# Kernel optimization log

Measured on AMD Instinct MI355X. Metric: run time of the kernel, lower is better.

The kernel has to match this reference:

```python
import jax, jax.numpy as jnp
import numpy as np

B, CIN, W = 4, 3, 28          # batch, in_channels, image size (= max_pos_embedding)
MID, HEADS, G, COUT = 16, 8, 4, 64
HALF = MID // 2               # row / col embedding dims


def _embed(u, w1, b1, gamma, beta, w2, b2):
    """Positional-embedding MLP applied elementwise to scalars u (N,).
    Conv2d(1->16,k=1) -> LayerNorm(16 channels) -> Swish -> Conv2d(16->MID/2,k=1)."""
    h = u[:, None] * w1[None, :] + b1                     # (N, 16)
    mu = h.mean(-1, keepdims=True)
    var = ((h - mu) ** 2).mean(-1, keepdims=True)
    h = gamma * (h - mu) / jnp.sqrt(var + 1e-5) + beta    # LayerNorm over channels
    h = h * jax.nn.sigmoid(h)                             # Swish
    return h @ w2.T + b2                                  # (N, HALF)


def _rot_indices():
    """Acted relative-position lookup indices for the 4 rotations.
    Values index into u = concat(rel, -rel) where rel = linspace(-1,1,2W-1)."""
    n = 2 * W - 1
    ar = np.arange(W)
    rel = ar[None, :] - ar[:, None] + (W - 1)             # rel[i,k] in [0, 2W-2]
    R = np.broadcast_to(rel[:, None, :, None], (W,) * 4)  # depends on (i,k)
    C = np.broadcast_to(rel[None, :, None, :], (W,) * 4)  # depends on (j,l)
    # rotation by 0/90/180/270 deg acting on (row, col) relative coordinates
    ridx = np.stack([R, C + n, R + n, C], 0)              # row component index
    cidx = np.stack([C, R, C + n, R + n], 0)              # col component index
    return jnp.asarray(ridx, jnp.int32), jnp.asarray(cidx, jnp.int32)


def setup_inputs() -> dict:
    key = jax.random.key(0)
    ks = jax.random.split(key, 24)
    def nrm(k, shape, fan):
        return jax.random.normal(k, shape, jnp.float32) / np.float32(np.sqrt(fan))
    inp = {"x": jax.random.normal(ks[0], (B, CIN, W, W), jnp.float32)}
    inp["wq"] = nrm(ks[1], (MID * HEADS, CIN), CIN); inp["bq"] = jnp.zeros((MID * HEADS,), jnp.float32)
    inp["wk"] = nrm(ks[2], (MID * HEADS, CIN), CIN); inp["bk"] = jnp.zeros((MID * HEADS,), jnp.float32)
    inp["wv"] = nrm(ks[3], (MID * HEADS, CIN), CIN); inp["bv"] = jnp.zeros((MID * HEADS,), jnp.float32)
    inp["w_out"] = nrm(ks[4], (COUT, MID * HEADS), MID * HEADS); inp["b_out"] = jnp.zeros((COUT,), jnp.float32)
    for pfx, base in (("row", 5), ("col", 12)):
        inp[f"{pfx}_w1"] = nrm(ks[base], (16,), 1)
        inp[f"{pfx}_b1"] = jnp.zeros((16,), jnp.float32)
        inp[f"{pfx}_gamma"] = jnp.ones((16,), jnp.float32)
        inp[f"{pfx}_beta"] = jnp.zeros((16,), jnp.float32)
        inp[f"{pfx}_w2"] = nrm(ks[base + 1], (HALF, 16), 16)
        inp[f"{pfx}_b2"] = jnp.zeros((HALF,), jnp.float32)
    inp["ridx"], inp["cidx"] = _rot_indices()
    return inp


def reference(x, wq, bq, wk, bk, wv, bv, w_out, b_out,
              row_w1, row_b1, row_gamma, row_beta, row_w2, row_b2,
              col_w1, col_b1, col_gamma, col_beta, col_w2, col_b2,
              ridx, cidx):
    b, c, H, Wd = x.shape
    # 1x1-conv q/k/v, viewed as (b, mid, heads, H, W)
    q = (jnp.einsum('oc,bcij->boij', wq, x) + bq[:, None, None]).reshape(b, MID, HEADS, H, Wd)
    k_ = (jnp.einsum('oc,bcij->boij', wk, x) + bk[:, None, None]).reshape(b, MID, HEADS, H, Wd)
    v = (jnp.einsum('oc,bcij->boij', wv, x) + bv[:, None, None]).reshape(b, MID, HEADS, H, Wd)

    content = jnp.einsum('bmhij,bmhkl->bhijkl', q, k_)     # (b,h,i,j,k,l)

    lin = jnp.linspace(-1.0, 1.0, 2 * Wd - 1)
    u = jnp.concatenate([lin, -lin])                       # unique relative coords
    E_row = _embed(u, row_w1, row_b1, row_gamma, row_beta, row_w2, row_b2)
    E_col = _embed(u, col_w1, col_b1, col_gamma, col_beta, col_w2, col_b2)
    row_emb = E_row[ridx]                                  # (G,i,j,k,l,HALF)
    col_emb = E_col[cidx]

    scores = jnp.einsum('bmhij,gijklm->bhgijkl', q[:, :HALF], row_emb)
    scores = scores + jnp.einsum('bmhij,gijklm->bhgijkl', q[:, HALF:], col_emb)
    scores = (scores + content[:, :, None]) / np.float32(np.sqrt(c))

    sh = scores.shape                                      # softmax over flattened (k,l)
    probs = jax.nn.softmax(scores.reshape(sh[:-2] + (-1,)), axis=-1).reshape(sh)

    out_v = jnp.einsum('bhgijkl,bmhkl->bmhgij', probs, v)  # (b,mid,heads,G,i,j)
    out_v = out_v.reshape(b, MID * HEADS, G, H, Wd)
    out = jnp.einsum('om,bmgij->bogij', w_out, out_v) + b_out[:, None, None, None]
    return out
```

## Files before the change

kernel.cpp:

```cpp
#include <hip/hip_runtime.h>
#include <hip/hip_fp16.h>

#define NPOS 784
#define WDIM 28

typedef _Float16 f16x8 __attribute__((ext_vector_type(8)));
typedef _Float16 f16x4 __attribute__((ext_vector_type(4)));
typedef float    f32x4 __attribute__((ext_vector_type(4)));

__global__ __launch_bounds__(256) void prep_kernel(
    const float* __restrict__ x,
    const float* __restrict__ wk, const float* __restrict__ bk,
    const float* __restrict__ wv, const float* __restrict__ bv,
    const float* __restrict__ w_out,
    const float* __restrict__ rw1, const float* __restrict__ rb1,
    const float* __restrict__ rga, const float* __restrict__ rbe,
    const float* __restrict__ rw2, const float* __restrict__ rb2,
    const float* __restrict__ cw1, const float* __restrict__ cb1,
    const float* __restrict__ cga, const float* __restrict__ cbe,
    const float* __restrict__ cw2, const float* __restrict__ cb2,
    _Float16* __restrict__ Kfrag, _Float16* __restrict__ Vfrag,
    _Float16* __restrict__ Wfrag, _Float16* __restrict__ Efrag)
{
    const int t = threadIdx.x;
    if (blockIdx.x == 416) {
        __shared__ float eb[1760];
        int d = -1, base = 0;
        const float *w1 = rw1, *b1 = rb1, *ga = rga, *be = rbe, *w2 = rw2, *b2 = rb2;
        if (t < 110) { d = t; }
        else if (t >= 128 && t < 238) { d = t - 128; base = 880; w1 = cw1; b1 = cb1; ga = cga; be = cbe; w2 = cw2; b2 = cb2; }
        if (d >= 0) {
            float u = (d < 55) ? (-1.0f + (float)d * (2.0f / 54.0f))
                               : -(-1.0f + (float)(d - 55) * (2.0f / 54.0f));
            float hb[16], mu = 0.0f;
#pragma unroll
            for (int c = 0; c < 16; ++c) { hb[c] = u * w1[c] + b1[c]; mu += hb[c]; }
            mu *= (1.0f / 16.0f);
            float var = 0.0f;
#pragma unroll
            for (int c = 0; c < 16; ++c) { float dv = hb[c] - mu; var += dv * dv; }
            var *= (1.0f / 16.0f);
            float rstd = rsqrtf(var + 1e-5f);
#pragma unroll
            for (int c = 0; c < 16; ++c) {
                float hn = ga[c] * (hb[c] - mu) * rstd + be[c];
                hb[c] = hn / (1.0f + __expf(-hn));
            }
#pragma unroll
            for (int m = 0; m < 8; ++m) {
                float e = b2[m];
#pragma unroll
                for (int c = 0; c < 16; ++c) e += hb[c] * w2[m * 16 + c];
                eb[base + m * 110 + d] = e;
            }
        }
        __syncthreads();
        for (int idx = t; idx < 1024; idx += 256) {
            int frag = idx >> 6, lane = idx & 63;
            int comp = frag >> 2, chunk = frag & 3;
            int dd = chunk * 16 + (lane & 15), kg = lane >> 4;
            f16x8 v = {};
            if (dd < 55) {
                int off = (comp & 2) ? dd + 55 : dd;
                if ((comp & 1) == 0 && kg == 0) {
#pragma unroll
                    for (int j = 0; j < 8; ++j) v[j] = (_Float16)eb[j * 110 + off];
                } else if ((comp & 1) == 1 && kg == 1) {
#pragma unroll
                    for (int j = 0; j < 8; ++j) v[j] = (_Float16)eb[880 + j * 110 + off];
                }
            }
            *(f16x8*)(Efrag + (size_t)idx * 8) = v;
        }
        return;
    }
    if (blockIdx.x == 417) {
        for (int idx = t; idx < 8192; idx += 256) {
            int obc = idx >> 9, lane = (idx >> 3) & 63, j = idx & 7;
            int o  = (obc >> 2) * 16 + (lane & 15);
            int mh = (obc & 3) * 32 + (lane >> 4) * 8 + j;
            Wfrag[idx] = (_Float16)w_out[o * 128 + mh];
        }
        return;
    }

    const int bid  = blockIdx.x;
    const int b    = bid / 104, rem = bid - b * 104;
    const int tile = rem >> 3, h = rem & 7;
    const int lane = t & 63, mg = t >> 6;
    const int bh   = b * 8 + h;

    {
        if (t < 128) {
            int sub = (t >> 5) & 3, l32 = 32 + (t & 31);
            int qz = tile * 4 + sub;
            if (qz < 49)
                *(f16x8*)(Kfrag + ((size_t)(bh * 49 + qz) * 64 + l32) * 8) = (f16x8){};
        }
        if (tile == 12 && t < 32)
            *(f16x8*)(Vfrag + ((size_t)(bh * 25 + 24) * 64 + 32 + t) * 8) = (f16x8){};
    }

    const int ij = tile * 64 + lane;
    if (ij >= NPOS) return;

    float x0 = x[(b * 3 + 0) * NPOS + ij];
    float x1 = x[(b * 3 + 1) * NPOS + ij];
    float x2 = x[(b * 3 + 2) * NPOS + ij];

    float4 kv;
    float vv[4];
#pragma unroll
    for (int j = 0; j < 4; ++j) {
        int m = mg * 4 + j, oc = m * 8 + h;
        float w0, w1, w2v;
        w0 = wk[oc*3+0]; w1 = wk[oc*3+1]; w2v = wk[oc*3+2];
        ((float*)&kv)[j] = bk[oc] + w0*x0 + w1*x1 + w2v*x2;
        w0 = wv[oc*3+0]; w1 = wv[oc*3+1]; w2v = wv[oc*3+2];
        vv[j] = bv[oc] + w0*x0 + w1*x1 + w2v*x2;
    }
    {
        int qt = ij >> 4;
        int lp = ((mg >> 1) << 4) | (ij & 15);
        int jb = (mg & 1) * 4;
        f16x4 k4 = {(_Float16)kv.x, (_Float16)kv.y, (_Float16)kv.z, (_Float16)kv.w};
        *(f16x4*)(Kfrag + ((size_t)(bh * 49 + qt) * 64 + lp) * 8 + jb) = k4;
    }
    {
        int s5 = ij >> 5, kk = ij & 31;
        _Float16* vb = Vfrag + (((size_t)(bh * 25 + s5) * 64 + ((kk >> 3) << 4)) << 3) + (kk & 7);
#pragma unroll
        for (int j = 0; j < 4; ++j) vb[(mg * 4 + j) * 8] = (_Float16)vv[j];
    }
}

#define UNI_OFF 56320
__global__ __launch_bounds__(512, 1) void attn_kernel(
    const _Float16* __restrict__ Kfrag, const _Float16* __restrict__ Vfrag,
    const _Float16* __restrict__ Wfrag, const _Float16* __restrict__ Efrag,
    const float* __restrict__ x,
    const float* __restrict__ wq, const float* __restrict__ bq,
    const float* __restrict__ b_out, float* __restrict__ out)
{
    __shared__ __align__(16) unsigned char smem[56320 + 82944];
    const int t = threadIdx.x, wave = t >> 6, lane = t & 63;
    const int q15 = lane & 15, rg = lane >> 4;

    int bid = blockIdx.x;
    int xcd = bid & 7;
    int lb  = ((xcd < 4) ? xcd * 25 : 100 + (xcd - 4) * 24) + (bid >> 3);
    const int b = lb / 49, qt = lb - b * 49;
    const int bh = b * 8 + wave;
    const int q_ij = qt * 16 + q15;
    const int iq = q_ij / WDIM, jq = q_ij % WDIM;
    const float c1 = 0.57735026918962576f * 1.44269504088896341f;

    float ql[8], qh[8];
    {
        float x0 = x[(b * 3 + 0) * NPOS + q_ij];
        float x1 = x[(b * 3 + 1) * NPOS + q_ij];
        float x2 = x[(b * 3 + 2) * NPOS + q_ij];
#pragma unroll
        for (int m = 0; m < 8; ++m) {
            int oc = m * 8 + wave;
            ql[m] = bq[oc] + wq[oc*3+0]*x0 + wq[oc*3+1]*x1 + wq[oc*3+2]*x2;
        }
#pragma unroll
        for (int m = 0; m < 8; ++m) {
            int oc = (m + 8) * 8 + wave;
            qh[m] = bq[oc] + wq[oc*3+0]*x0 + wq[oc*3+1]*x1 + wq[oc*3+2]*x2;
        }
    }
    f16x8 qf = {};
    if (rg == 0) {
#pragma unroll
        for (int j = 0; j < 8; ++j) qf[j] = (_Float16)ql[j];
    } else if (rg == 1) {
#pragma unroll
        for (int j = 0; j < 8; ++j) qf[j] = (_Float16)qh[j];
    }

    {
        const f16x8* efr = (const f16x8*)Efrag;
        float tm0 = -3.0e38f, tm1 = -3.0e38f, tm2 = -3.0e38f, tm3 = -3.0e38f;
#pragma unroll
        for (int chunk = 0; chunk < 4; ++chunk) {
            f32x4 Dr  = __builtin_amdgcn_mfma_f32_16x16x32_f16(efr[(0*4+chunk)*64+lane], qf, (f32x4){0,0,0,0}, 0, 0, 0);
            f32x4 Dc  = __builtin_amdgcn_mfma_f32_16x16x32_f16(efr[(1*4+chunk)*64+lane], qf, (f32x4){0,0,0,0}, 0, 0, 0);
            f32x4 D5r = __builtin_amdgcn_mfma_f32_16x16x32_f16(efr[(2*4+chunk)*64+lane], qf, (f32x4){0,0,0,0}, 0, 0, 0);
            f32x4 D5c = __builtin_amdgcn_mfma_f32_16x16x32_f16(efr[(3*4+chunk)*64+lane], qf, (f32x4){0,0,0,0}, 0, 0, 0);
#pragma unroll
            for (int reg = 0; reg < 4; ++reg) {
                int dd = chunk * 16 + rg * 4 + reg;
                if (dd < 55) {
                    tm0 = fmaxf(tm0, Dr[reg]);  tm1 = fmaxf(tm1, Dc[reg]);
                    tm2 = fmaxf(tm2, D5r[reg]); tm3 = fmaxf(tm3, D5c[reg]);
                }
            }
        }
        tm0 = fmaxf(tm0, __shfl_xor(tm0, 16, 64)); tm0 = fmaxf(tm0, __shfl_xor(tm0, 32, 64));
        tm1 = fmaxf(tm1, __shfl_xor(tm1, 16, 64)); tm1 = fmaxf(tm1, __shfl_xor(tm1, 32, 64));
        tm2 = fmaxf(tm2, __shfl_xor(tm2, 16, 64)); tm2 = fmaxf(tm2, __shfl_xor(tm2, 32, 64));
        tm3 = fmaxf(tm3, __shfl_xor(tm3, 16, 64)); tm3 = fmaxf(tm3, __shfl_xor(tm3, 32, 64));
        uint2* tabw = (uint2*)smem + (wave * 16 + q15) * 55;
#pragma unroll
        for (int chunk = 0; chunk < 4; ++chunk) {
            f32x4 Dr  = __builtin_amdgcn_mfma_f32_16x16x32_f16(efr[(0*4+chunk)*64+lane], qf, (f32x4){0,0,0,0}, 0, 0, 0);
            f32x4 Dc  = __builtin_amdgcn_mfma_f32_16x16x32_f16(efr[(1*4+chunk)*64+lane], qf, (f32x4){0,0,0,0}, 0, 0, 0);
            f32x4 D5r = __builtin_amdgcn_mfma_f32_16x16x32_f16(efr[(2*4+chunk)*64+lane], qf, (f32x4){0,0,0,0}, 0, 0, 0);
            f32x4 D5c = __builtin_amdgcn_mfma_f32_16x16x32_f16(efr[(3*4+chunk)*64+lane], qf, (f32x4){0,0,0,0}, 0, 0, 0);
#pragma unroll
            for (int reg = 0; reg < 4; ++reg) {
                int dd = chunk * 16 + rg * 4 + reg;
                if (dd < 55) {
                    __half2 h01 = __floats2half2_rn(exp2f(c1 * (Dr[reg]  - tm0)),
                                                    exp2f(c1 * (Dc[reg]  - tm1)));
                    __half2 h23 = __floats2half2_rn(exp2f(c1 * (D5r[reg] - tm2)),
                                                    exp2f(c1 * (D5c[reg] - tm3)));
                    uint2 w; w.x = *(unsigned int*)&h01; w.y = *(unsigned int*)&h23;
                    tabw[dd] = w;
                }
            }
        }
    }

    const f16x8* kchunk = (const f16x8*)(Kfrag + (size_t)bh * 49 * 64 * 8);

    float mx = -3.0e38f;
#pragma unroll 7
    for (int ch = 0; ch < 49; ++ch) {
        f16x8 kf = kchunk[ch * 64 + lane];
        f32x4 s = __builtin_amdgcn_mfma_f32_16x16x32_f16(kf, qf, (f32x4){0,0,0,0}, 0, 0, 0);
        mx = fmaxf(mx, fmaxf(fmaxf(s[0], s[1]), fmaxf(s[2], s[3])));
    }
    mx = fmaxf(mx, __shfl_xor(mx, 16, 64));
    mx = fmaxf(mx, __shfl_xor(mx, 32, 64));
    const float c2f = 6.0f - mx * c1;

    f32x4 d0 = {0,0,0,0}, d1 = {0,0,0,0}, d2 = {0,0,0,0}, d3 = {0,0,0,0};
    f32x4 e0 = {0,0,0,0}, e1 = {0,0,0,0}, e2 = {0,0,0,0}, e3 = {0,0,0,0};
    _Float16* ptw = (_Float16*)(smem + UNI_OFF) + (size_t)wave * 5184;
    const uint2* tab = (const uint2*)smem + (wave * 16 + q15) * 55;
    const int prow  = (q15 & 3) * 4;
    const int tbase = (q15 >> 2) * 648;
    const int rof   = q15 * 40 + rg * 8;
    const f16x8* vbase = (const f16x8*)(Vfrag + (size_t)bh * 25 * 64 * 8);
    f16x8 onesB;
#pragma unroll
    for (int j = 0; j < 8; ++j) onesB[j] = (_Float16)1.0f;

    f16x8 kfA = kchunk[0 * 64 + lane];
    f16x8 kfB = kchunk[1 * 64 + lane];
    f16x8 bfCur = vbase[lane];
    f16x8 bfPrev = {};
    for (int pv = 0; pv < 25; ++pv) {
        _Float16*       wbuf = ptw + (pv & 1) * 2592;
        const _Float16* rbuf = ptw + ((pv & 1) ^ 1) * 2592;
        f16x8 aA = *(const f16x8*)(rbuf + 0 * 648 + rof);
        f16x8 aB = *(const f16x8*)(rbuf + 1 * 648 + rof);
        f16x8 aC = *(const f16x8*)(rbuf + 2 * 648 + rof);
        f16x8 aD = *(const f16x8*)(rbuf + 3 * 648 + rof);
        int nA = (pv * 2 + 2 < 49) ? pv * 2 + 2 : 48;
        int nB = (pv * 2 + 3 < 49) ? pv * 2 + 3 : 48;
        int nV = (pv + 1 < 25) ? pv + 1 : 24;
        f16x8 kfA2 = kchunk[nA * 64 + lane];
        f16x8 kfB2 = kchunk[nB * 64 + lane];
        f16x8 bf2  = vbase[nV * 64 + lane];
#pragma unroll
        for (int c2 = 0; c2 < 2; ++c2) {
            int ch = pv * 2 + c2;
            int cb = rg * 4 + c2 * 16;
            if (ch < 49) {
                f16x8 kf = c2 ? kfB : kfA;
                f32x4 s = __builtin_amdgcn_mfma_f32_16x16x32_f16(kf, qf, (f32x4){0,0,0,0}, 0, 0, 0);
                float pg[4][4];
#pragma unroll
                for (int reg = 0; reg < 4; ++reg) {
                    float ec = exp2f(s[reg] * c1 + c2f);
                    int k = ch * 16 + rg * 4 + reg;
                    int rk = (k * 2341) >> 16;
                    int ck = k - rk * WDIM;
                    uint2 tr = tab[rk - iq + 27];
                    uint2 tc = tab[ck - jq + 27];
                    float2 r01 = __half22float2(*(__half2*)&tr.x);
                    float2 r23 = __half22float2(*(__half2*)&tr.y);
                    float2 c01 = __half22float2(*(__half2*)&tc.x);
                    float2 c23 = __half22float2(*(__half2*)&tc.y);
                    pg[0][reg] = ec * r01.x * c01.y;
                    pg[1][reg] = ec * r01.y * c23.x;
                    pg[2][reg] = ec * r23.x * c23.y;
                    pg[3][reg] = ec * r23.y * c01.x;
                }
#pragma unroll
                for (int g = 0; g < 4; ++g) {
                    __half2 a01 = __floats2half2_rn(pg[g][0], pg[g][1]);
                    __half2 a23 = __floats2half2_rn(pg[g][2], pg[g][3]);
                    uint2 w; w.x = *(unsigned int*)&a01; w.y = *(unsigned int*)&a23;
                    *(uint2*)(wbuf + tbase + (prow + g) * 40 + cb) = w;
                }
            } else {
                uint2 w; w.x = 0u; w.y = 0u;
#pragma unroll
                for (int g = 0; g < 4; ++g)
                    *(uint2*)(wbuf + tbase + (prow + g) * 40 + cb) = w;
            }
        }
        if (pv) {
            __builtin_amdgcn_s_setprio(1);
            d0 = __builtin_amdgcn_mfma_f32_16x16x32_f16(aA, bfPrev, d0, 0, 0, 0);
            e0 = __builtin_amdgcn_mfma_f32_16x16x32_f16(aA, onesB,  e0, 0, 0, 0);
            d1 = __builtin_amdgcn_mfma_f32_16x16x32_f16(aB, bfPrev, d1, 0, 0, 0);
            e1 = __builtin_amdgcn_mfma_f32_16x16x32_f16(aB, onesB,  e1, 0, 0, 0);
            d2 = __builtin_amdgcn_mfma_f32_16x16x32_f16(aC, bfPrev, d2, 0, 0, 0);
            e2 = __builtin_amdgcn_mfma_f32_16x16x32_f16(aC, onesB,  e2, 0, 0, 0);
            d3 = __builtin_amdgcn_mfma_f32_16x16x32_f16(aD, bfPrev, d3, 0, 0, 0);
            e3 = __builtin_amdgcn_mfma_f32_16x16x32_f16(aD, onesB,  e3, 0, 0, 0);
            __builtin_amdgcn_s_setprio(0);
        }
        kfA = kfA2; kfB = kfB2; bfPrev = bfCur; bfCur = bf2;
    }
    {
        const _Float16* rbuf = ptw;
        f16x8 aA = *(const f16x8*)(rbuf + 0 * 648 + rof);
        f16x8 aB = *(const f16x8*)(rbuf + 1 * 648 + rof);
        f16x8 aC = *(const f16x8*)(rbuf + 2 * 648 + rof);
        f16x8 aD = *(const f16x8*)(rbuf + 3 * 648 + rof);
        __builtin_amdgcn_s_setprio(1);
        d0 = __builtin_amdgcn_mfma_f32_16x16x32_f16(aA, bfPrev, d0, 0, 0, 0);
        e0 = __builtin_amdgcn_mfma_f32_16x16x32_f16(aA, onesB,  e0, 0, 0, 0);
        d1 = __builtin_amdgcn_mfma_f32_16x16x32_f16(aB, bfPrev, d1, 0, 0, 0);
        e1 = __builtin_amdgcn_mfma_f32_16x16x32_f16(aB, onesB,  e1, 0, 0, 0);
        d2 = __builtin_amdgcn_mfma_f32_16x16x32_f16(aC, bfPrev, d2, 0, 0, 0);
        e2 = __builtin_amdgcn_mfma_f32_16x16x32_f16(aC, onesB,  e2, 0, 0, 0);
        d3 = __builtin_amdgcn_mfma_f32_16x16x32_f16(aD, bfPrev, d3, 0, 0, 0);
        e3 = __builtin_amdgcn_mfma_f32_16x16x32_f16(aD, onesB,  e3, 0, 0, 0);
        __builtin_amdgcn_s_setprio(0);
    }

    __syncthreads();
    _Float16* ovh = (_Float16*)(smem + UNI_OFF);
    {
        int mo = q15 * 8 + wave;
#pragma unroll
        for (int reg = 0; reg < 4; ++reg) {
            float i0 = (e0[reg] > 0.0f) ? 1.0f / e0[reg] : 0.0f;
            float i1 = (e1[reg] > 0.0f) ? 1.0f / e1[reg] : 0.0f;
            float i2 = (e2[reg] > 0.0f) ? 1.0f / e2[reg] : 0.0f;
            float i3 = (e3[reg] > 0.0f) ? 1.0f / e3[reg] : 0.0f;
            ovh[(reg * 16 +      rg) * 136 + mo] = (_Float16)(d0[reg] * i0);
            ovh[(reg * 16 +  4 + rg) * 136 + mo] = (_Float16)(d1[reg] * i1);
            ovh[(reg * 16 +  8 + rg) * 136 + mo] = (_Float16)(d2[reg] * i2);
            ovh[(reg * 16 + 12 + rg) * 136 + mo] = (_Float16)(d3[reg] * i3);
        }
    }
    __syncthreads();

#pragma unroll
    for (int tt2 = 0; tt2 < 2; ++tt2) {
        int tl = wave * 2 + tt2;
        int ob = tl >> 2, g = tl & 3;
        f32x4 dd = {0,0,0,0};
#pragma unroll
        for (int c = 0; c < 4; ++c) {
            f16x8 wa = *(const f16x8*)(Wfrag + ((size_t)((ob * 4 + c) * 64 + lane)) * 8);
            f16x8 vb = *(const f16x8*)(ovh + (g * 16 + q15) * 136 + c * 32 + rg * 8);
            dd = __builtin_amdgcn_mfma_f32_16x16x32_f16(wa, vb, dd, 0, 0, 0);
        }
#pragma unroll
        for (int reg = 0; reg < 4; ++reg) {
            int o = ob * 16 + rg * 4 + reg;
            out[((size_t)(b * 64 + o) * 4 + g) * NPOS + qt * 16 + q15] = dd[reg] + b_out[o];
        }
    }
}

extern "C" void kernel_launch(void* const* d_in, const int* in_sizes, int n_in,
                              void* d_out, int out_size, void* d_ws, size_t ws_size,
                              hipStream_t stream)
{
    const float* x     = (const float*)d_in[0];
    const float* wq    = (const float*)d_in[1];
    const float* bq    = (const float*)d_in[2];
    const float* wk    = (const float*)d_in[3];
    const float* bk    = (const float*)d_in[4];
    const float* wv    = (const float*)d_in[5];
    const float* bv    = (const float*)d_in[6];
    const float* w_out = (const float*)d_in[7];
    const float* b_out = (const float*)d_in[8];
    const float* rw1 = (const float*)d_in[9];
    const float* rb1 = (const float*)d_in[10];
    const float* rga = (const float*)d_in[11];
    const float* rbe = (const float*)d_in[12];
    const float* rw2 = (const float*)d_in[13];
    const float* rb2 = (const float*)d_in[14];
    const float* cw1 = (const float*)d_in[15];
    const float* cb1 = (const float*)d_in[16];
    const float* cga = (const float*)d_in[17];
    const float* cbe = (const float*)d_in[18];
    const float* cw2 = (const float*)d_in[19];
    const float* cb2 = (const float*)d_in[20];

    _Float16* Kfrag  = (_Float16*)d_ws;
    _Float16* Vfrag  = Kfrag + 802816;
    _Float16* Wfrag  = Vfrag + 409600;
    _Float16* Efrag  = Wfrag + 8192;

    prep_kernel<<<418, 256, 0, stream>>>(x, wk, bk, wv, bv, w_out,
                                         rw1, rb1, rga, rbe, rw2, rb2,
                                         cw1, cb1, cga, cbe, cw2, cb2,
                                         Kfrag, Vfrag, Wfrag, Efrag);
    attn_kernel<<<196, 512, 0, stream>>>(Kfrag, Vfrag, Wfrag, Efrag,
                                         x, wq, bq, b_out, (float*)d_out);
}
```

Measured before the change: 148.9 us.

## Replace two-pass softmax max with online rescaling and single-buffer P tile

Removes the separate pass that computed the row maximum over all 49 key chunks, and instead keeps a running max with online-softmax rescaling of the accumulators on each pair of chunks. The P tile in LDS goes from double-buffered to single-buffered, and the PV MFMAs now run in the same iteration right after P is written. This saves 49 MFMAs plus K reloads per wave. In exchange it adds shuffles, exp2 and accumulator rescales every iteration, and it loses the overlap between writing P and consuming the previous P.

```diff
diff --git a/kernel.cpp b/kernel.cpp
--- a/kernel.cpp
+++ b/kernel.cpp
@@ -226,20 +226,10 @@
 
     const f16x8* kchunk = (const f16x8*)(Kfrag + (size_t)bh * 49 * 64 * 8);
 
-    float mx = -3.0e38f;
-#pragma unroll 7
-    for (int ch = 0; ch < 49; ++ch) {
-        f16x8 kf = kchunk[ch * 64 + lane];
-        f32x4 s = __builtin_amdgcn_mfma_f32_16x16x32_f16(kf, qf, (f32x4){0,0,0,0}, 0, 0, 0);
-        mx = fmaxf(mx, fmaxf(fmaxf(s[0], s[1]), fmaxf(s[2], s[3])));
-    }
-    mx = fmaxf(mx, __shfl_xor(mx, 16, 64));
-    mx = fmaxf(mx, __shfl_xor(mx, 32, 64));
-    const float c2f = 6.0f - mx * c1;
-
     f32x4 d0 = {0,0,0,0}, d1 = {0,0,0,0}, d2 = {0,0,0,0}, d3 = {0,0,0,0};
     f32x4 e0 = {0,0,0,0}, e1 = {0,0,0,0}, e2 = {0,0,0,0}, e3 = {0,0,0,0};
-    _Float16* ptw = (_Float16*)(smem + UNI_OFF) + (size_t)wave * 5184;
+    float m_cur = -3.0e38f;
+    _Float16* ptw = (_Float16*)(smem + UNI_OFF) + (size_t)wave * 2592;
     const uint2* tab = (const uint2*)smem + (wave * 16 + q15) * 55;
     const int prow  = (q15 & 3) * 4;
     const int tbase = (q15 >> 2) * 648;
@@ -252,31 +242,42 @@
     f16x8 kfA = kchunk[0 * 64 + lane];
     f16x8 kfB = kchunk[1 * 64 + lane];
     f16x8 bfCur = vbase[lane];
-    f16x8 bfPrev = {};
     for (int pv = 0; pv < 25; ++pv) {
-        _Float16*       wbuf = ptw + (pv & 1) * 2592;
-        const _Float16* rbuf = ptw + ((pv & 1) ^ 1) * 2592;
-        f16x8 aA = *(const f16x8*)(rbuf + 0 * 648 + rof);
-        f16x8 aB = *(const f16x8*)(rbuf + 1 * 648 + rof);
-        f16x8 aC = *(const f16x8*)(rbuf + 2 * 648 + rof);
-        f16x8 aD = *(const f16x8*)(rbuf + 3 * 648 + rof);
         int nA = (pv * 2 + 2 < 49) ? pv * 2 + 2 : 48;
         int nB = (pv * 2 + 3 < 49) ? pv * 2 + 3 : 48;
         int nV = (pv + 1 < 25) ? pv + 1 : 24;
         f16x8 kfA2 = kchunk[nA * 64 + lane];
         f16x8 kfB2 = kchunk[nB * 64 + lane];
         f16x8 bf2  = vbase[nV * 64 + lane];
+
+        f32x4 sA = __builtin_amdgcn_mfma_f32_16x16x32_f16(kfA, qf, (f32x4){0,0,0,0}, 0, 0, 0);
+        f32x4 sB = __builtin_amdgcn_mfma_f32_16x16x32_f16(kfB, qf, (f32x4){0,0,0,0}, 0, 0, 0);
+
+        float mloc = fmaxf(fmaxf(fmaxf(sA[0], sA[1]), fmaxf(sA[2], sA[3])),
+                           fmaxf(fmaxf(sB[0], sB[1]), fmaxf(sB[2], sB[3])));
+        mloc = fmaxf(mloc, __shfl_xor(mloc, 16, 64));
+        mloc = fmaxf(mloc, __shfl_xor(mloc, 32, 64));
+        float m_new = fmaxf(m_cur, mloc);
+        float sc = exp2f(c1 * (m_cur - m_new));
+        float sc0 = __shfl(sc, rg, 64);
+        float sc1 = __shfl(sc, 4 + rg, 64);
+        float sc2 = __shfl(sc, 8 + rg, 64);
+        float sc3 = __shfl(sc, 12 + rg, 64);
+        d0 *= sc0; e0 *= sc0; d1 *= sc1; e1 *= sc1;
+        d2 *= sc2; e2 *= sc2; d3 *= sc3; e3 *= sc3;
+        m_cur = m_new;
+        const float c2d = 6.0f - m_new * c1;
+
 #pragma unroll
         for (int c2 = 0; c2 < 2; ++c2) {
             int ch = pv * 2 + c2;
             int cb = rg * 4 + c2 * 16;
             if (ch < 49) {
-                f16x8 kf = c2 ? kfB : kfA;
-                f32x4 s = __builtin_amdgcn_mfma_f32_16x16x32_f16(kf, qf, (f32x4){0,0,0,0}, 0, 0, 0);
+                f32x4 s = c2 ? sB : sA;
                 float pg[4][4];
 #pragma unroll
                 for (int reg = 0; reg < 4; ++reg) {
-                    float ec = exp2f(s[reg] * c1 + c2f);
+                    float ec = exp2f(s[reg] * c1 + c2d);
                     int k = ch * 16 + rg * 4 + reg;
                     int rk = (k * 2341) >> 16;
                     int ck = k - rk * WDIM;
@@ -296,45 +297,30 @@
                     __half2 a01 = __floats2half2_rn(pg[g][0], pg[g][1]);
                     __half2 a23 = __floats2half2_rn(pg[g][2], pg[g][3]);
                     uint2 w; w.x = *(unsigned int*)&a01; w.y = *(unsigned int*)&a23;
-                    *(uint2*)(wbuf + tbase + (prow + g) * 40 + cb) = w;
+                    *(uint2*)(ptw + tbase + (prow + g) * 40 + cb) = w;
                 }
             } else {
                 uint2 w; w.x = 0u; w.y = 0u;
 #pragma unroll
                 for (int g = 0; g < 4; ++g)
-                    *(uint2*)(wbuf + tbase + (prow + g) * 40 + cb) = w;
-            }
-        }
-        if (pv) {
-            __builtin_amdgcn_s_setprio(1);
-            d0 = __builtin_amdgcn_mfma_f32_16x16x32_f16(aA, bfPrev, d0, 0, 0, 0);
-            e0 = __builtin_amdgcn_mfma_f32_16x16x32_f16(aA, onesB,  e0, 0, 0, 0);
-            d1 = __builtin_amdgcn_mfma_f32_16x16x32_f16(aB, bfPrev, d1, 0, 0, 0);
-            e1 = __builtin_amdgcn_mfma_f32_16x16x32_f16(aB, onesB,  e1, 0, 0, 0);
-            d2 = __builtin_amdgcn_mfma_f32_16x16x32_f16(aC, bfPrev, d2, 0, 0, 0);
-            e2 = __builtin_amdgcn_mfma_f32_16x16x32_f16(aC, onesB,  e2, 0, 0, 0);
-            d3 = __builtin_amdgcn_mfma_f32_16x16x32_f16(aD, bfPrev, d3, 0, 0, 0);
-            e3 = __builtin_amdgcn_mfma_f32_16x16x32_f16(aD, onesB,  e3, 0, 0, 0);
-            __builtin_amdgcn_s_setprio(0);
-        }
-        kfA = kfA2; kfB = kfB2; bfPrev = bfCur; bfCur = bf2;
-    }
-    {
-        const _Float16* rbuf = ptw;
-        f16x8 aA = *(const f16x8*)(rbuf + 0 * 648 + rof);
-        f16x8 aB = *(const f16x8*)(rbuf + 1 * 648 + rof);
-        f16x8 aC = *(const f16x8*)(rbuf + 2 * 648 + rof);
-        f16x8 aD = *(const f16x8*)(rbuf + 3 * 648 + rof);
+                    *(uint2*)(ptw + tbase + (prow + g) * 40 + cb) = w;
+            }
+        }
+        f16x8 aA = *(const f16x8*)(ptw + 0 * 648 + rof);
+        f16x8 aB = *(const f16x8*)(ptw + 1 * 648 + rof);
+        f16x8 aC = *(const f16x8*)(ptw + 2 * 648 + rof);
+        f16x8 aD = *(const f16x8*)(ptw + 3 * 648 + rof);
         __builtin_amdgcn_s_setprio(1);
-        d0 = __builtin_amdgcn_mfma_f32_16x16x32_f16(aA, bfPrev, d0, 0, 0, 0);
-        e0 = __builtin_amdgcn_mfma_f32_16x16x32_f16(aA, onesB,  e0, 0, 0, 0);
-        d1 = __builtin_amdgcn_mfma_f32_16x16x32_f16(aB, bfPrev, d1, 0, 0, 0);
-        e1 = __builtin_amdgcn_mfma_f32_16x16x32_f16(aB, onesB,  e1, 0, 0, 0);
-        d2 = __builtin_amdgcn_mfma_f32_16x16x32_f16(aC, bfPrev, d2, 0, 0, 0);
-        e2 = __builtin_amdgcn_mfma_f32_16x16x32_f16(aC, onesB,  e2, 0, 0, 0);
-        d3 = __builtin_amdgcn_mfma_f32_16x16x32_f16(aD, bfPrev, d3, 0, 0, 0);
-        e3 = __builtin_amdgcn_mfma_f32_16x16x32_f16(aD, onesB,  e3, 0, 0, 0);
+        d0 = __builtin_amdgcn_mfma_f32_16x16x32_f16(aA, bfCur, d0, 0, 0, 0);
+        e0 = __builtin_amdgcn_mfma_f32_16x16x32_f16(aA, onesB, e0, 0, 0, 0);
+        d1 = __builtin_amdgcn_mfma_f32_16x16x32_f16(aB, bfCur, d1, 0, 0, 0);
+        e1 = __builtin_amdgcn_mfma_f32_16x16x32_f16(aB, onesB, e1, 0, 0, 0);
+        d2 = __builtin_amdgcn_mfma_f32_16x16x32_f16(aC, bfCur, d2, 0, 0, 0);
+        e2 = __builtin_amdgcn_mfma_f32_16x16x32_f16(aC, onesB, e2, 0, 0, 0);
+        d3 = __builtin_amdgcn_mfma_f32_16x16x32_f16(aD, bfCur, d3, 0, 0, 0);
+        e3 = __builtin_amdgcn_mfma_f32_16x16x32_f16(aD, onesB, e3, 0, 0, 0);
         __builtin_amdgcn_s_setprio(0);
+        kfA = kfA2; kfB = kfB2; bfCur = bf2;
     }
 
     __syncthreads();
```

Result: no change. 149.8 us (+0.6%).
